# Performance work log

Hardware: AMD Instinct MI355X
Metric: run time of the kernel (lower is better)

## Reference

```python
import jax, jax.numpy as jnp
import numpy as np

B, T, C = 16, 2048, 128
HEAD_SIZE = 128

def setup_inputs() -> dict:
    key = jax.random.key(0)
    k1, k2, k3, k4 = jax.random.split(key, 4)
    x = jax.random.normal(k1, (B, T, C), dtype=jnp.float32)
    # nn.Linear(N_EMBED, head_size, bias=False) weight shape: [head_size, N_EMBED]
    scale = (1.0 / np.sqrt(C)).astype(np.float32)
    Wq = jax.random.normal(k2, (HEAD_SIZE, C), dtype=jnp.float32) * scale
    Wk = jax.random.normal(k3, (HEAD_SIZE, C), dtype=jnp.float32) * scale
    Wv = jax.random.normal(k4, (HEAD_SIZE, C), dtype=jnp.float32) * scale
    return {"x": x, "Wq": Wq, "Wk": Wk, "Wv": Wv}

def reference(x, Wq, Wk, Wv):
    Bd, Td, Cd = x.shape
    q = jnp.einsum('btc,hc->bth', x, Wq)  # [B,T,H]
    k = jnp.einsum('btc,hc->bth', x, Wk)
    v = jnp.einsum('btc,hc->bth', x, Wv)
    # NOTE: original scales by C**-0.5 (embedding dim), not head_size**-0.5
    scores = jnp.einsum('bth,bsh->bts', q, k) * (Cd ** -0.5)  # [B,T,T]
    causal = jnp.tril(jnp.ones((Td, Td), dtype=bool))
    scores = jnp.where(causal, scores, -jnp.inf)
    attn = jax.nn.softmax(scores, axis=-1)
    out = jnp.einsum('bts,bsh->bth', attn, v)  # [B,T,H]
    return out
```

## Files before the change

### kernel.cpp

```cpp
#include <hip/hip_runtime.h>
#include <hip/hip_bf16.h>

#define BB 16
#define TT 2048
#define CC 128
#define HH 128
#define NQT128 16

typedef __bf16 bf16x8 __attribute__((ext_vector_type(8)));
typedef float  f32x4  __attribute__((ext_vector_type(4)));

#define BTH       ((size_t)BB * TT * HH)
#define WBF_OFF   (3 * BTH)
#define PARTIAL_OFF_BYTES (3 * BTH * 2 + 3 * 128 * 128 * 2)
#define SLOT_BYTES 33280
#define SLOT_L_OFF 32768

static __device__ __forceinline__ bf16x8 load_cvt8(const float* p) {
    float4 a = *(const float4*)p;
    float4 b = *(const float4*)(p + 4);
    bf16x8 r;
    r[0] = (__bf16)a.x; r[1] = (__bf16)a.y; r[2] = (__bf16)a.z; r[3] = (__bf16)a.w;
    r[4] = (__bf16)b.x; r[5] = (__bf16)b.y; r[6] = (__bf16)b.z; r[7] = (__bf16)b.w;
    return r;
}

static __device__ __forceinline__ void load_lds16(const void* g, void* l) {
    __builtin_amdgcn_global_load_lds(
        (const __attribute__((address_space(1))) unsigned int*)g,
        (__attribute__((address_space(3))) unsigned int*)l, 16, 0, 0);
}

#define BAR_VM()   asm volatile("s_waitcnt vmcnt(0)\n\ts_barrier" ::: "memory")
#define BAR_LGKM() asm volatile("s_waitcnt lgkmcnt(0)\n\ts_barrier" ::: "memory")

__global__ __launch_bounds__(256) void wcvt_kernel(
    const float* __restrict__ Wq, const float* __restrict__ Wk,
    const float* __restrict__ Wv, __bf16* __restrict__ wbf)
{
    int idx = blockIdx.x * 256 + threadIdx.x;
    int which = idx >> 11;
    int rem = idx & 2047;
    int blk = rem >> 8;
    int r2  = rem & 255;
    int ks   = r2 >> 6;
    int lane = r2 & 63;
    int quad = lane >> 4, l16 = lane & 15;
    const float* src = (which == 0) ? Wq : (which == 1) ? Wk : Wv;
    float sc = (which == 0) ? (0.08838834764831845f * 1.4426950408889634f) : 1.0f;
    const float* p = src + (size_t)(blk * 16 + l16) * CC + ks * 32 + quad * 8;
    bf16x8 v;
    #pragma unroll
    for (int j = 0; j < 8; ++j) v[j] = (__bf16)(p[j] * sc);
    *(bf16x8*)(wbf + (size_t)which * 16384 + (((size_t)(blk * 4 + ks)) << 9) + lane * 8) = v;
}

#define TR_QK 132
#define TR_V  68

__global__ __launch_bounds__(256) void proj_kernel(
    const float* __restrict__ x, __bf16* __restrict__ ws)
{
    __shared__ float  xs[64 * 132];
    __shared__ __bf16 tr[128 * TR_V];

    const int lane = threadIdx.x & 63;
    const int wave = threadIdx.x >> 6;
    const int quad = lane >> 4;
    const int l16  = lane & 15;
    const int tid  = threadIdx.x;
    const int m0 = blockIdx.x * 64;
    const int b  = m0 / TT;
    const int t0 = m0 % TT;

    const __bf16* Wbf = ws + WBF_OFF;
    __bf16* Qs = ws;
    __bf16* Ks = ws + BTH;
    __bf16* Vs = ws + 2 * BTH;

    const float* xg = x + (size_t)m0 * CC;
    #pragma unroll
    for (int t = 0; t < 8; ++t) {
        int f = t * 256 + tid;
        int row = f >> 5, c4 = f & 31;
        float4 v = *(const float4*)(xg + (size_t)f * 4);
        *(float4*)(&xs[row * 132 + c4 * 4]) = v;
    }
    __syncthreads();

    bf16x8 xf[4];
    #pragma unroll
    for (int ks = 0; ks < 4; ++ks)
        xf[ks] = load_cvt8(&xs[(wave * 16 + l16) * 132 + ks * 32 + quad * 8]);

    #pragma unroll
    for (int which = 0; which < 2; ++which) {
        const __bf16* Wb = Wbf + (size_t)which * 16384;
        __bf16* dst = which ? Ks : Qs;
        #pragma unroll
        for (int nt = 0; nt < 8; ++nt) {
            f32x4 acc = {0.f, 0.f, 0.f, 0.f};
            #pragma unroll
            for (int ks = 0; ks < 4; ++ks) {
                bf16x8 wf = *(const bf16x8*)(Wb + (((size_t)(nt * 4 + ks)) << 9) + lane * 8);
                acc = __builtin_amdgcn_mfma_f32_16x16x32_bf16(xf[ks], wf, acc, 0, 0, 0);
            }
            #pragma unroll
            for (int r = 0; r < 4; ++r)
                tr[(wave * 16 + quad * 4 + r) * TR_QK + nt * 16 + l16] = (__bf16)acc[r];
        }
        asm volatile("s_waitcnt lgkmcnt(0)" ::: "memory");
        #pragma unroll
        for (int ks = 0; ks < 4; ++ks) {
            const __bf16* p = &tr[(wave * 16 + l16) * TR_QK + ks * 32 + quad * 8];
            uint2 lo = *(const uint2*)p;
            uint2 hi = *(const uint2*)(p + 4);
            uint4 v; v.x = lo.x; v.y = lo.y; v.z = hi.x; v.w = hi.y;
            __bf16* o = dst + (((size_t)(b * 128 + t0 / 16 + wave) * 4 + ks) << 9) + lane * 8;
            *(uint4*)o = v;
        }
        asm volatile("s_waitcnt lgkmcnt(0)" ::: "memory");
    }

    __syncthreads();
    const __bf16* Wv = Wbf + 2 * 16384;
    #pragma unroll
    for (int msub = 0; msub < 8; ++msub) {
        f32x4 acc = {0.f, 0.f, 0.f, 0.f};
        #pragma unroll
        for (int ks = 0; ks < 4; ++ks) {
            bf16x8 wf = *(const bf16x8*)(Wv + (((size_t)(msub * 4 + ks)) << 9) + lane * 8);
            acc = __builtin_amdgcn_mfma_f32_16x16x32_bf16(wf, xf[ks], acc, 0, 0, 0);
        }
        #pragma unroll
        for (int r = 0; r < 4; ++r)
            tr[(msub * 16 + quad * 4 + r) * TR_V + wave * 16 + l16] = (__bf16)acc[r];
    }
    __syncthreads();
    #pragma unroll
    for (int i = 0; i < 4; ++i) {
        int t32 = i >> 1;
        int h16 = wave * 2 + (i & 1);
        const __bf16* p = &tr[(h16 * 16 + l16) * TR_V + t32 * 32 + quad * 8];
        uint2 lo = *(const uint2*)p;
        uint2 hi = *(const uint2*)(p + 4);
        uint4 v; v.x = lo.x; v.y = lo.y; v.z = hi.x; v.w = hi.y;
        __bf16* o = Vs + (((size_t)(b * 64 + t0 / 32 + t32) * 8 + h16) << 9) + lane * 8;
        *(uint4*)o = v;
    }
}

#define S_LDS 76
#define EXP_BIAS 16.0f

__global__ __launch_bounds__(256) void attn_kernel(
    const __bf16* __restrict__ ws, char* __restrict__ po,
    float* __restrict__ outp, int G, int SPB, int direct)
{
    __shared__ __bf16 ldsK[8192];
    __shared__ __bf16 ldsV[8192];
    __shared__ __bf16 lds_p[4 * 32 * S_LDS];

    const int lane = threadIdx.x & 63;
    const int wave = threadIdx.x >> 6;
    const int quad = lane >> 4;
    const int l16  = lane & 15;
    const int lane8 = lane * 8;

    const int lin = blockIdx.x;
    const int b  = (lin & 7) * 2 + ((lin >> 3) & 1);
    const int s  = SPB - 1 - (lin >> 4);

    int acc = 0, qt = 0, seg = 0;
    for (int q = 0; q < NQT128; ++q) {
        int c = (2 * (q + 1) + G - 1) / G;
        if (s < acc + c) { qt = q; seg = s - acc; break; }
        acc += c;
    }
    const int kt0 = seg * G;
    int kt1 = 2 * (qt + 1);
    if (kt0 + G < kt1) kt1 = kt0 + G;
    const int segs_qt = (2 * (qt + 1) + G - 1) / G;
    const int dwrite = direct | (segs_qt == 1);

    const int qw = qt * 128 + wave * 32;
    int kt1w = (qw + 32 + 63) >> 6;
    if (kt1w > kt1) kt1w = kt1;

    const __bf16* Qs = ws;
    const __bf16* Ks = ws + BTH;
    const __bf16* Vs = ws + 2 * BTH;

    bf16x8 qf[2][4];
    #pragma unroll
    for (int m = 0; m < 2; ++m)
        #pragma unroll
        for (int ks = 0; ks < 4; ++ks)
            qf[m][ks] = *(const bf16x8*)(Qs + (((size_t)(b * 128 + qt * 8 + wave * 2 + m) * 4 + ks) << 9) + lane8);

    float l_r[2][4];
    f32x4 o[2][8];
    #pragma unroll
    for (int m = 0; m < 2; ++m) {
        #pragma unroll
        for (int r = 0; r < 4; ++r) l_r[m][r] = 0.f;
        #pragma unroll
        for (int h8 = 0; h8 < 8; ++h8) o[m][h8] = (f32x4){0.f, 0.f, 0.f, 0.f};
    }

    __bf16* myP = lds_p + wave * 32 * S_LDS;

    #define STAGE_K(KT)                                                             \
        do {                                                                        \
            const char* kb_ = (const char*)(Ks + (((size_t)(b * 128 + (KT) * 4) * 4) << 9)); \
            _Pragma("unroll")                                                       \
            for (int i_ = 0; i_ < 4; ++i_) {                                        \
                int c_ = wave * 4 + i_;                                             \
                load_lds16(kb_ + c_ * 1024 + (size_t)lane * 16, (char*)ldsK + c_ * 1024); \
            }                                                                       \
        } while (0)
    #define STAGE_V(KT)                                                             \
        do {                                                                        \
            const char* vb_ = (const char*)(Vs + (((size_t)(b * 64 + (KT) * 2) * 8) << 9)); \
            _Pragma("unroll")                                                       \
            for (int i_ = 0; i_ < 4; ++i_) {                                        \
                int c_ = wave * 4 + i_;                                             \
                load_lds16(vb_ + c_ * 1024 + (size_t)lane * 16, (char*)ldsV + c_ * 1024); \
            }                                                                       \
        } while (0)

    STAGE_K(kt0);
    STAGE_V(kt0);

    for (int kt = kt0; kt < kt1; ++kt) {
        BAR_VM();

        f32x4 s2[2][4];
        if (kt < kt1w) {
            #pragma unroll
            for (int nsub = 0; nsub < 4; ++nsub) {
                bf16x8 kfr[4];
                #pragma unroll
                for (int ks = 0; ks < 4; ++ks)
                    kfr[ks] = *(const bf16x8*)((const char*)ldsK + ((nsub * 4 + ks) << 10) + lane * 16);
                #pragma unroll
                for (int m = 0; m < 2; ++m) {
                    f32x4 a2 = {0.f, 0.f, 0.f, 0.f};
                    #pragma unroll
                    for (int ks = 0; ks < 4; ++ks)
                        a2 = __builtin_amdgcn_mfma_f32_16x16x32_bf16(qf[m][ks], kfr[ks], a2, 0, 0, 0);
                    s2[m][nsub] = a2;
                }
            }
        }
        BAR_LGKM();
        if (kt + 1 < kt1) STAGE_K(kt + 1);

        if (kt < kt1w) {
            const int k0 = kt * 64;
            #pragma unroll
            for (int m = 0; m < 2; ++m) {
                const int qr0m = qw + m * 16;
                if (k0 + 63 > qr0m) {
                    #pragma unroll
                    for (int nsub = 0; nsub < 4; ++nsub) {
                        int key = k0 + nsub * 16 + l16;
                        #pragma unroll
                        for (int r = 0; r < 4; ++r) {
                            int rowq = qr0m + quad * 4 + r;
                            if (key > rowq) s2[m][nsub][r] = -3e38f;
                        }
                    }
                }
                #pragma unroll
                for (int nsub = 0; nsub < 4; ++nsub) {
                    #pragma unroll
                    for (int r = 0; r < 4; ++r) {
                        float p = __builtin_amdgcn_exp2f(s2[m][nsub][r] - EXP_BIAS);
                        l_r[m][r] += p;
                        myP[(m * 16 + quad * 4 + r) * S_LDS + nsub * 16 + l16] = (__bf16)p;
                    }
                }
            }
            asm volatile("s_waitcnt lgkmcnt(0)" ::: "memory");

            bf16x8 pf[2][2];
            #pragma unroll
            for (int m = 0; m < 2; ++m)
                #pragma unroll
                for (int ks2 = 0; ks2 < 2; ++ks2) {
                    union { bf16x8 v; uint2 h[2]; } u;
                    const char* base = (const char*)myP + (size_t)(m * 16 + l16) * (S_LDS * 2) + ks2 * 64 + quad * 16;
                    u.h[0] = *(const uint2*)base;
                    u.h[1] = *(const uint2*)(base + 8);
                    pf[m][ks2] = u.v;
                }

            #pragma unroll
            for (int h8 = 0; h8 < 8; ++h8) {
                bf16x8 v0 = *(const bf16x8*)((const char*)ldsV + ((0 * 8 + h8) << 10) + lane * 16);
                bf16x8 v1 = *(const bf16x8*)((const char*)ldsV + ((1 * 8 + h8) << 10) + lane * 16);
                #pragma unroll
                for (int m = 0; m < 2; ++m) {
                    o[m][h8] = __builtin_amdgcn_mfma_f32_16x16x32_bf16(pf[m][0], v0, o[m][h8], 0, 0, 0);
                    o[m][h8] = __builtin_amdgcn_mfma_f32_16x16x32_bf16(pf[m][1], v1, o[m][h8], 0, 0, 0);
                }
            }
        }
        BAR_LGKM();
        if (kt + 1 < kt1) STAGE_V(kt + 1);
    }

    #pragma unroll
    for (int m = 0; m < 2; ++m)
        #pragma unroll
        for (int r = 0; r < 4; ++r)
            #pragma unroll
            for (int j = 1; j <= 8; j <<= 1)
                l_r[m][r] += __shfl_xor(l_r[m][r], j, 64);

    if (dwrite) {
        #pragma unroll
        for (int m = 0; m < 2; ++m) {
            float inv[4];
            #pragma unroll
            for (int r = 0; r < 4; ++r) inv[r] = 1.0f / l_r[m][r];
            #pragma unroll
            for (int h8 = 0; h8 < 8; ++h8)
                #pragma unroll
                for (int r = 0; r < 4; ++r)
                    outp[(size_t)(b * TT + qw + m * 16 + quad * 4 + r) * HH + h8 * 16 + l16] = o[m][h8][r] * inv[r];
        }
    } else {
        char* slot = po + (size_t)(b * SPB + s) * SLOT_BYTES;
        __bf16* slot_o = (__bf16*)slot;
        float*  slot_l = (float*)(slot + SLOT_L_OFF);
        #pragma unroll
        for (int m = 0; m < 2; ++m) {
            #pragma unroll
            for (int h8 = 0; h8 < 8; ++h8)
                #pragma unroll
                for (int r = 0; r < 4; ++r)
                    slot_o[(size_t)(wave * 32 + m * 16 + quad * 4 + r) * 128 + h8 * 16 + l16] = (__bf16)o[m][h8][r];
            if (l16 == 0) {
                #pragma unroll
                for (int r = 0; r < 4; ++r)
                    slot_l[wave * 32 + m * 16 + quad * 4 + r] = l_r[m][r];
            }
        }
    }
}

__global__ __launch_bounds__(256) void reduce_kernel(
    const char* __restrict__ po, float* __restrict__ outp, int G, int SPB)
{
    __shared__ float lsum[32];
    const int qt  = blockIdx.x >> 2;
    const int qtr = blockIdx.x & 3;
    const int b   = blockIdx.y;
    const int tid = threadIdx.x;

    const int segs = (2 * (qt + 1) + G - 1) / G;
    if (segs == 1) return;

    int acc = 0;
    for (int qq = 0; qq < qt; ++qq) acc += (2 * (qq + 1) + G - 1) / G;
    const char* base = po + (size_t)(b * SPB + acc) * SLOT_BYTES;
    const int r0 = qtr * 32;

    if (tid < 32) {
        float v = 0.f;
        for (int sg = 0; sg < segs; ++sg)
            v += ((const float*)(base + (size_t)sg * SLOT_BYTES + SLOT_L_OFF))[r0 + tid];
        lsum[tid] = v;
    }
    __syncthreads();

    const int rsub = tid >> 4;
    const int cg   = tid & 15;
    float a[2][8];
    #pragma unroll
    for (int p = 0; p < 2; ++p)
        #pragma unroll
        for (int j = 0; j < 8; ++j) a[p][j] = 0.f;

    for (int sg = 0; sg < segs; ++sg) {
        const char* sb = base + (size_t)sg * SLOT_BYTES;
        #pragma unroll
        for (int p = 0; p < 2; ++p) {
            int row = r0 + rsub + p * 16;
            union { uint4 u; __bf16 h[8]; } v;
            v.u = *(const uint4*)(sb + ((size_t)row * 128 + cg * 8) * 2);
            #pragma unroll
            for (int j = 0; j < 8; ++j) a[p][j] += (float)v.h[j];
        }
    }

    #pragma unroll
    for (int p = 0; p < 2; ++p) {
        int row = r0 + rsub + p * 16;
        float inv = 1.0f / lsum[rsub + p * 16];
        float* op = outp + (size_t)(b * TT + qt * 128 + row) * HH + cg * 8;
        float4 o0 = {a[p][0] * inv, a[p][1] * inv, a[p][2] * inv, a[p][3] * inv};
        float4 o1 = {a[p][4] * inv, a[p][5] * inv, a[p][6] * inv, a[p][7] * inv};
        *(float4*)op = o0;
        *(float4*)(op + 4) = o1;
    }
}

extern "C" void kernel_launch(void* const* d_in, const int* in_sizes, int n_in,
                              void* d_out, int out_size, void* d_ws, size_t ws_size,
                              hipStream_t stream)
{
    const float* x  = (const float*)d_in[0];
    const float* Wq = (const float*)d_in[1];
    const float* Wk = (const float*)d_in[2];
    const float* Wv = (const float*)d_in[3];
    __bf16* ws = (__bf16*)d_ws;
    float* out = (float*)d_out;
    char* po   = (char*)d_ws + PARTIAL_OFF_BYTES;

    int G = 0, SPB = 0, direct = 1;
    const int cand[3] = {6, 8, 16};
    for (int ci = 0; ci < 3; ++ci) {
        int g = cand[ci], spb = 0;
        for (int q = 0; q < NQT128; ++q) spb += (2 * (q + 1) + g - 1) / g;
        size_t need = PARTIAL_OFF_BYTES + (size_t)spb * BB * SLOT_BYTES;
        if (need <= ws_size) { G = g; SPB = spb; direct = 0; break; }
    }
    if (direct) { G = 2 * NQT128; SPB = NQT128; }

    wcvt_kernel<<<24, 256, 0, stream>>>(Wq, Wk, Wv, ws + WBF_OFF);
    proj_kernel<<<512, 256, 0, stream>>>(x, ws);
    attn_kernel<<<SPB * 16, 256, 0, stream>>>(ws, po, out, G, SPB, direct);
    if (!direct) {
        dim3 rgrid(NQT128 * 4, BB);
        reduce_kernel<<<rgrid, 256, 0, stream>>>(po, out, G, SPB);
    }
}
```

Baseline: 143.4 us.

## Double-buffer K/V tiles with 32-key steps in attention kernel

```diff
diff --git a/kernel.cpp b/kernel.cpp
--- a/kernel.cpp
+++ b/kernel.cpp
@@ -150,16 +150,16 @@
     }
 }
 
-#define S_LDS 76
+#define S32 40
 #define EXP_BIAS 16.0f
 
 __global__ __launch_bounds__(256) void attn_kernel(
     const __bf16* __restrict__ ws, char* __restrict__ po,
     float* __restrict__ outp, int G, int SPB, int direct)
 {
-    __shared__ __bf16 ldsK[8192];
-    __shared__ __bf16 ldsV[8192];
-    __shared__ __bf16 lds_p[4 * 32 * S_LDS];
+    __shared__ __bf16 ldsK[2][4096];
+    __shared__ __bf16 ldsV[2][4096];
+    __shared__ __bf16 lds_p[4 * 32 * S32];
 
     const int lane = threadIdx.x & 63;
     const int wave = threadIdx.x >> 6;
@@ -183,9 +183,10 @@
     const int segs_qt = (2 * (qt + 1) + G - 1) / G;
     const int dwrite = direct | (segs_qt == 1);
 
+    const int tt0 = kt0 * 2, tt1 = kt1 * 2;
     const int qw = qt * 128 + wave * 32;
-    int kt1w = (qw + 32 + 63) >> 6;
-    if (kt1w > kt1) kt1w = kt1;
+    int ttw = (qw + 63) >> 5;
+    if (ttw > tt1) ttw = tt1;
 
     const __bf16* Qs = ws;
     const __bf16* Ks = ws + BTH;
@@ -208,41 +209,38 @@
         for (int h8 = 0; h8 < 8; ++h8) o[m][h8] = (f32x4){0.f, 0.f, 0.f, 0.f};
     }
 
-    __bf16* myP = lds_p + wave * 32 * S_LDS;
-
-    #define STAGE_K(KT)                                                             \
+    __bf16* myP = lds_p + wave * 32 * S32;
+
+    #define STAGE32(TTv, BUF)                                                       \
         do {                                                                        \
-            const char* kb_ = (const char*)(Ks + (((size_t)(b * 128 + (KT) * 4) * 4) << 9)); \
+            const char* kb_ = (const char*)(Ks + (((size_t)(b * 128 + (TTv) * 2) * 4) << 9)); \
+            const char* vb_ = (const char*)(Vs + (((size_t)(b * 64 + (TTv)) * 8) << 9));      \
             _Pragma("unroll")                                                       \
-            for (int i_ = 0; i_ < 4; ++i_) {                                        \
-                int c_ = wave * 4 + i_;                                             \
-                load_lds16(kb_ + c_ * 1024 + (size_t)lane * 16, (char*)ldsK + c_ * 1024); \
+            for (int i_ = 0; i_ < 2; ++i_) {                                        \
+                int c_ = wave * 2 + i_;                                             \
+                load_lds16(kb_ + c_ * 1024 + (size_t)lane * 16, (char*)ldsK[BUF] + c_ * 1024); \
+                load_lds16(vb_ + c_ * 1024 + (size_t)lane * 16, (char*)ldsV[BUF] + c_ * 1024); \
             }                                                                       \
         } while (0)
-    #define STAGE_V(KT)                                                             \
-        do {                                                                        \
-            const char* vb_ = (const char*)(Vs + (((size_t)(b * 64 + (KT) * 2) * 8) << 9)); \
-            _Pragma("unroll")                                                       \
-            for (int i_ = 0; i_ < 4; ++i_) {                                        \
-                int c_ = wave * 4 + i_;                                             \
-                load_lds16(vb_ + c_ * 1024 + (size_t)lane * 16, (char*)ldsV + c_ * 1024); \
-            }                                                                       \
-        } while (0)
-
-    STAGE_K(kt0);
-    STAGE_V(kt0);
-
-    for (int kt = kt0; kt < kt1; ++kt) {
+
+    STAGE32(tt0, 0);
+
+    for (int tt = tt0; tt < tt1; ++tt) {
+        const int cur = (tt - tt0) & 1;
         BAR_VM();
-
-        f32x4 s2[2][4];
-        if (kt < kt1w) {
-            #pragma unroll
-            for (int nsub = 0; nsub < 4; ++nsub) {
+        if (tt + 1 < tt1) STAGE32(tt + 1, cur ^ 1);
+
+        if (tt < ttw) {
+            const char* lk = (const char*)ldsK[cur];
+            const char* lv = (const char*)ldsV[cur];
+
+            f32x4 s2[2][2];
+            #pragma unroll
+            for (int nsub = 0; nsub < 2; ++nsub) {
                 bf16x8 kfr[4];
                 #pragma unroll
                 for (int ks = 0; ks < 4; ++ks)
-                    kfr[ks] = *(const bf16x8*)((const char*)ldsK + ((nsub * 4 + ks) << 10) + lane * 16);
+                    kfr[ks] = *(const bf16x8*)(lk + ((nsub * 4 + ks) << 10) + lane * 16);
                 #pragma unroll
                 for (int m = 0; m < 2; ++m) {
                     f32x4 a2 = {0.f, 0.f, 0.f, 0.f};
@@ -252,18 +250,14 @@
                     s2[m][nsub] = a2;
                 }
             }
-        }
-        BAR_LGKM();
-        if (kt + 1 < kt1) STAGE_K(kt + 1);
-
-        if (kt < kt1w) {
-            const int k0 = kt * 64;
+
+            const int k0 = tt * 32;
             #pragma unroll
             for (int m = 0; m < 2; ++m) {
                 const int qr0m = qw + m * 16;
-                if (k0 + 63 > qr0m) {
+                if (k0 + 31 > qr0m) {
                     #pragma unroll
-                    for (int nsub = 0; nsub < 4; ++nsub) {
+                    for (int nsub = 0; nsub < 2; ++nsub) {
                         int key = k0 + nsub * 16 + l16;
                         #pragma unroll
                         for (int r = 0; r < 4; ++r) {
@@ -273,42 +267,31 @@
                     }
                 }
                 #pragma unroll
-                for (int nsub = 0; nsub < 4; ++nsub) {
+                for (int nsub = 0; nsub < 2; ++nsub) {
                     #pragma unroll
                     for (int r = 0; r < 4; ++r) {
                         float p = __builtin_amdgcn_exp2f(s2[m][nsub][r] - EXP_BIAS);
                         l_r[m][r] += p;
-                        myP[(m * 16 + quad * 4 + r) * S_LDS + nsub * 16 + l16] = (__bf16)p;
+                        myP[(m * 16 + quad * 4 + r) * S32 + nsub * 16 + l16] = (__bf16)p;
                     }
                 }
             }
             asm volatile("s_waitcnt lgkmcnt(0)" ::: "memory");
 
-            bf16x8 pf[2][2];
+            bf16x8 pf[2];
             #pragma unroll
             for (int m = 0; m < 2; ++m)
-                #pragma unroll
-                for (int ks2 = 0; ks2 < 2; ++ks2) {
-                    union { bf16x8 v; uint2 h[2]; } u;
-                    const char* base = (const char*)myP + (size_t)(m * 16 + l16) * (S_LDS * 2) + ks2 * 64 + quad * 16;
-                    u.h[0] = *(const uint2*)base;
-                    u.h[1] = *(const uint2*)(base + 8);
-                    pf[m][ks2] = u.v;
-                }
+                pf[m] = *(const bf16x8*)((const char*)myP + (size_t)(m * 16 + l16) * (S32 * 2) + quad * 16);
 
             #pragma unroll
             for (int h8 = 0; h8 < 8; ++h8) {
-                bf16x8 v0 = *(const bf16x8*)((const char*)ldsV + ((0 * 8 + h8) << 10) + lane * 16);
-                bf16x8 v1 = *(const bf16x8*)((const char*)ldsV + ((1 * 8 + h8) << 10) + lane * 16);
-                #pragma unroll
-                for (int m = 0; m < 2; ++m) {
-                    o[m][h8] = __builtin_amdgcn_mfma_f32_16x16x32_bf16(pf[m][0], v0, o[m][h8], 0, 0, 0);
-                    o[m][h8] = __builtin_amdgcn_mfma_f32_16x16x32_bf16(pf[m][1], v1, o[m][h8], 0, 0, 0);
-                }
+                bf16x8 v0 = *(const bf16x8*)(lv + (h8 << 10) + lane * 16);
+                #pragma unroll
+                for (int m = 0; m < 2; ++m)
+                    o[m][h8] = __builtin_amdgcn_mfma_f32_16x16x32_bf16(pf[m], v0, o[m][h8], 0, 0, 0);
             }
         }
         BAR_LGKM();
-        if (kt + 1 < kt1) STAGE_V(kt + 1);
     }
 
     #pragma unroll
```

New measurement: 135.4 us. -5.5%, faster.
